# Kernel optimization log

Measured on AMD Instinct MI355X. Metric: run time of the kernel, lower is better.

## Reference

```python
import jax, jax.numpy as jnp
import numpy as np

NEG = -1e30  # log-space 'zero' (avoids -inf NaN issues under jit)
EPS = 1e-7   # keras.backend.epsilon()


def _ctc_loss(y_true, y_pred):
    # y_true: [B, L] int labels in [0, C-1), y_pred: [B, T, C] softmax probs.
    # Keras ctc_batch_cost: logits = log(y_pred + eps), then tf.nn.ctc_loss
    # (which applies log_softmax internally), blank = C - 1.
    B, T, C = y_pred.shape
    L = y_true.shape[1]
    S = 2 * L + 1
    blank = C - 1

    logp = jax.nn.log_softmax(jnp.log(y_pred + EPS), axis=-1)  # [B, T, C]

    # Extended label sequence: blank, l1, blank, l2, ..., blank  -> [B, S]
    ext = jnp.full((B, S), blank, dtype=y_true.dtype).at[:, 1::2].set(y_true)
    lp_ext = jnp.take_along_axis(logp, ext[:, None, :].astype(jnp.int32), axis=2)  # [B, T, S]

    # skip transition s-2 -> s allowed iff ext[s] != blank and ext[s] != ext[s-2]
    ext_m2 = jnp.concatenate([jnp.full((B, 2), blank, ext.dtype), ext[:, :-2]], axis=1)
    allow_skip = (ext != blank) & (ext != ext_m2)
    allow_skip = allow_skip.at[:, :2].set(False)

    # alpha init at t=0
    alpha = jnp.full((B, S), NEG, dtype=logp.dtype)
    alpha = alpha.at[:, 0].set(lp_ext[:, 0, 0]).at[:, 1].set(lp_ext[:, 0, 1])

    neg1 = jnp.full((B, 1), NEG, dtype=logp.dtype)
    neg2 = jnp.full((B, 2), NEG, dtype=logp.dtype)

    def step(a, lp_t):
        prev1 = jnp.concatenate([neg1, a[:, :-1]], axis=1)
        prev2 = jnp.concatenate([neg2, a[:, :-2]], axis=1)
        acc = jnp.logaddexp(a, prev1)
        acc = jnp.where(allow_skip, jnp.logaddexp(acc, prev2), acc)
        return acc + lp_t, None

    lp_seq = jnp.transpose(lp_ext, (1, 0, 2))[1:]  # [T-1, B, S]
    alpha, _ = jax.lax.scan(step, alpha, lp_seq)

    loss = -jnp.logaddexp(alpha[:, -1], alpha[:, -2])  # [B]
    return loss[:, None]  # [B, 1] like keras ctc_batch_cost


def setup_inputs() -> dict:
    key = jax.random.key(0)
    k1, k2 = jax.random.split(key)
    B, T, C, L = 1024, 256, 128, 64
    y_true = jax.random.randint(k1, (B, L), 0, C - 1, dtype=jnp.int32)
    y_pred = jax.random.uniform(k2, (B, T, C), dtype=jnp.float32, minval=1e-4, maxval=1.0)
    return {"y_true": y_true, "y_pred": y_pred}


def reference(y_true, y_pred):
    return _ctc_loss(y_true, y_pred)
```

## Files before the change

kernel.cpp:

```cpp
#include <hip/hip_runtime.h>
#include <math.h>

#define BATCH 1024
#define TT    256
#define CC    128
#define LL    64
#define EPSV  (1e-7f)

typedef float f32x4 __attribute__((ext_vector_type(4)));

template <int CTRL>
__device__ __forceinline__ float dpp0(float x) {
    return __int_as_float(__builtin_amdgcn_update_dpp(0, __float_as_int(x), CTRL, 0xF, 0xF, true));
}
template <int CTRL>
__device__ __forceinline__ float dppS(float x) {
    return __int_as_float(__builtin_amdgcn_update_dpp(__float_as_int(x), __float_as_int(x), CTRL, 0xF, 0xF, false));
}
__device__ __forceinline__ float rol1_f(float x) {
    return __int_as_float(__builtin_amdgcn_update_dpp(__float_as_int(x), __float_as_int(x), 0x134, 0xF, 0xF, false));
}
__device__ __forceinline__ int rol1_i(int x) {
    return __builtin_amdgcn_update_dpp(x, x, 0x134, 0xF, 0xF, false);
}
__device__ __forceinline__ float rdlane(float x, int l) {
    return __int_as_float(__builtin_amdgcn_readlane(__float_as_int(x), l));
}
__device__ __forceinline__ float wave_max_bcast(float m) {
    m = fmaxf(m, dppS<0x111>(m));
    m = fmaxf(m, dppS<0x112>(m));
    m = fmaxf(m, dppS<0x114>(m));
    m = fmaxf(m, dppS<0x118>(m));
    m = fmaxf(m, dppS<0x142>(m));
    m = fmaxf(m, dppS<0x143>(m));
    return rdlane(m, 63);
}
__device__ __forceinline__ unsigned f2h(float x) {
    _Float16 h = (_Float16)x;
    unsigned short u; __builtin_memcpy(&u, &h, 2);
    return (unsigned)u;
}
__device__ __forceinline__ float h2f(unsigned short u) {
    _Float16 h; __builtin_memcpy(&h, &u, 2);
    return (float)h;
}

__global__ __launch_bounds__(512, 8) void ctc_fwd_kernel(const int* __restrict__ y_true,
                                                         const float* __restrict__ y_pred,
                                                         float* __restrict__ out) {
    __shared__ unsigned short qtab[TT][66];
    __shared__ float qblank[TT];
    __shared__ float logZpart[8];

    const int b    = blockIdx.x;
    const int tid  = threadIdx.x;
    const int wv   = tid >> 6;
    const int lane = tid & 63;

    const float* yp = y_pred + (size_t)b * (TT * CC);
    const int lab  = y_true[b * LL + lane];
    const int srcA = lab >> 2;
    const int srcB = 32 + srcA;
    const bool hiPair = (lab & 2) != 0;
    const bool hiHalf = (lab & 1) != 0;

    const int off = ((lane >> 5) << 7) + ((lane & 31) << 2);
    const float* base = yp + off;

    float zacc = 0.0f;
    f32x4 v[4];
    #pragma unroll
    for (int j = 0; j < 4; ++j)
        v[j] = __builtin_nontemporal_load((const f32x4*)(base + 256 * (wv + 8 * j)));

    for (int g = 0; g < 4; ++g) {
        f32x4 vn[4];
        if (g < 3) {
            #pragma unroll
            for (int j = 0; j < 4; ++j)
                vn[j] = __builtin_nontemporal_load((const f32x4*)(base + 256 * (wv + 32 * (g + 1) + 8 * j)));
        }
        #pragma unroll
        for (int j = 0; j < 4; ++j) {
            const int r2 = wv + 32 * g + 8 * j;
            const int tA = 2 * r2, tB = tA + 1;
            float q0 = v[j][0] + EPSV, q1 = v[j][1] + EPSV;
            float q2 = v[j][2] + EPSV, q3 = v[j][3] + EPSV;
            float s = (q0 + q1) + (q2 + q3);
            s += dpp0<0x111>(s);
            s += dpp0<0x112>(s);
            s += dpp0<0x114>(s);
            s += dpp0<0x118>(s);
            s += dpp0<0x142>(s);
            zacc += __logf(s);
            int i01 = (int)(f2h(q0) | (f2h(q1) << 16));
            int i23 = (int)(f2h(q2) | (f2h(q3) << 16));
            int gA01 = __shfl(i01, srcA), gA23 = __shfl(i23, srcA);
            int gB01 = __shfl(i01, srcB), gB23 = __shfl(i23, srcB);
            int sA = hiPair ? gA23 : gA01;
            int sB = hiPair ? gB23 : gB01;
            qtab[tA][lane] = (unsigned short)(hiHalf ? ((unsigned)sA >> 16) : (sA & 0xFFFF));
            qtab[tB][lane] = (unsigned short)(hiHalf ? ((unsigned)sB >> 16) : (sB & 0xFFFF));
            if ((lane & 31) == 31) qblank[tA + (lane >> 5)] = q3;
        }
        #pragma unroll
        for (int j = 0; j < 4; ++j) v[j] = vn[j];
    }
    {
        float z31 = rdlane(zacc, 31), z63 = rdlane(zacc, 63);
        if (lane == 0) logZpart[wv] = z31 + z63;
    }
    __syncthreads();

    if (wv == 0) {
        float logZ = 0.0f;
        #pragma unroll
        for (int w = 0; w < 8; ++w) logZ += logZpart[w];

        const int labm1  = rol1_i(lab);
        const float mskip = (lane >= 1 && lab != labm1) ? 1.0f : 0.0f;
        const bool l0 = (lane == 0);

        float a0 = l0 ? qblank[0] : 0.0f;
        float a1 = l0 ? h2f(qtab[0][lane]) : 0.0f;
        float aX = 0.0f;
        int Esum = 0;

        float qbv[8], qlv[8];
        #pragma unroll
        for (int i = 0; i < 8; ++i) {
            qbv[i] = qblank[1 + i];
            qlv[i] = h2f(qtab[1 + i][lane]);
        }

        for (int t0 = 1; t0 + 8 <= TT; t0 += 8) {
            float qbn[8], qln[8];
            #pragma unroll
            for (int i = 0; i < 8; ++i) {
                int tn = t0 + 8 + i; tn = (tn < TT) ? tn : (TT - 1);
                qbn[i] = qblank[tn];
                qln[i] = h2f(qtab[tn][lane]);
            }
            #pragma unroll
            for (int i = 0; i < 8; ++i) {
                float nb  = rol1_f(a1);
                float na0 = (a0 + (l0 ? 0.0f : nb)) * qbv[i];
                float na1 = fmaf(mskip, nb, a0 + a1) * qlv[i];
                aX = l0 ? (aX + nb) * qbv[i] : 0.0f;
                a0 = na0; a1 = na1;
            }
            float m = fmaxf(fmaxf(a0, a1), aX);
            float mall = wave_max_bcast(m);
            int ex = (int)((__float_as_uint(mall) >> 23) & 0xFF);
            int e  = 127 - ex;
            float sc = __uint_as_float((unsigned)(127 + e) << 23);
            a0 *= sc; a1 *= sc; aX *= sc;
            Esum += e;
            #pragma unroll
            for (int i = 0; i < 8; ++i) { qbv[i] = qbn[i]; qlv[i] = qln[i]; }
        }
        #pragma unroll
        for (int i = 0; i < 7; ++i) {
            float nb  = rol1_f(a1);
            float na0 = (a0 + (l0 ? 0.0f : nb)) * qbv[i];
            float na1 = fmaf(mskip, nb, a0 + a1) * qlv[i];
            aX = l0 ? (aX + nb) * qbv[i] : 0.0f;
            a0 = na0; a1 = na1;
        }
        float a127 = rdlane(a1, 63);
        if (lane == 0) {
            float tot = aX + a127;
            out[b] = logZ + (float)Esum * 0.69314718055994531f - __logf(tot);
        }
    }
}

extern "C" void kernel_launch(void* const* d_in, const int* in_sizes, int n_in,
                              void* d_out, int out_size, void* d_ws, size_t ws_size,
                              hipStream_t stream) {
    const int*   y_true = (const int*)d_in[0];
    const float* y_pred = (const float*)d_in[1];
    float*       out    = (float*)d_out;
    ctc_fwd_kernel<<<BATCH, 512, 0, stream>>>(y_true, y_pred, out);
}
```

Before: 37.38 us.

## Overlap CTC recursion with producer waves via LDS chunk counters

Makes wave 0 a dedicated consumer that runs the alpha recursion while waves 1-7 load y_pred, build the fp16 label-probability table and signal per-chunk completion through LDS atomic counters. Wave 0 spins on each 8-timestep chunk instead of waiting at one block-wide barrier, so the serial recursion starts before the load phase finishes. It also swaps the per-element fp16 conversion for packed cvt_pkrtz. The risks are spin-wait overhead, relying on LDS ordering through waitcnt and atomics, one fewer loading wave, and round-toward-zero conversion changing rounding slightly.

```diff
diff --git a/kernel.cpp b/kernel.cpp
--- a/kernel.cpp
+++ b/kernel.cpp
@@ -8,6 +8,7 @@
 #define EPSV  (1e-7f)
 
 typedef float f32x4 __attribute__((ext_vector_type(4)));
+typedef __fp16 fp16x2 __attribute__((ext_vector_type(2)));
 
 template <int CTRL>
 __device__ __forceinline__ float dpp0(float x) {
@@ -35,10 +36,10 @@
     m = fmaxf(m, dppS<0x143>(m));
     return rdlane(m, 63);
 }
-__device__ __forceinline__ unsigned f2h(float x) {
-    _Float16 h = (_Float16)x;
-    unsigned short u; __builtin_memcpy(&u, &h, 2);
-    return (unsigned)u;
+__device__ __forceinline__ int pkrtz(float a, float b) {
+    fp16x2 h = __builtin_amdgcn_cvt_pkrtz(a, b);
+    int r; __builtin_memcpy(&r, &h, 4);
+    return r;
 }
 __device__ __forceinline__ float h2f(unsigned short u) {
     _Float16 h; __builtin_memcpy(&h, &u, 2);
@@ -51,6 +52,8 @@
     __shared__ unsigned short qtab[TT][66];
     __shared__ float qblank[TT];
     __shared__ float logZpart[8];
+    __shared__ int   chunkCnt[32];
+    __shared__ int   doneCnt;
 
     const int b    = blockIdx.x;
     const int tid  = threadIdx.x;
@@ -67,110 +70,124 @@
     const int off = ((lane >> 5) << 7) + ((lane & 31) << 2);
     const float* base = yp + off;
 
-    float zacc = 0.0f;
-    f32x4 v[4];
-    #pragma unroll
-    for (int j = 0; j < 4; ++j)
-        v[j] = __builtin_nontemporal_load((const f32x4*)(base + 256 * (wv + 8 * j)));
-
-    for (int g = 0; g < 4; ++g) {
-        f32x4 vn[4];
-        if (g < 3) {
-            #pragma unroll
-            for (int j = 0; j < 4; ++j)
-                vn[j] = __builtin_nontemporal_load((const f32x4*)(base + 256 * (wv + 32 * (g + 1) + 8 * j)));
-        }
+    if (tid < 32) chunkCnt[tid] = 0;
+    if (tid == 32) doneCnt = 0;
+    __syncthreads();
+
+    if (wv > 0) {
+        const int sw = wv - 1;
+        float zacc = 0.0f;
+        f32x4 v[8];
         #pragma unroll
-        for (int j = 0; j < 4; ++j) {
-            const int r2 = wv + 32 * g + 8 * j;
+        for (int d = 0; d < 8; ++d) {
+            int r2 = sw + 7 * d; r2 = (r2 < 128) ? r2 : 127;
+            v[d] = *(const f32x4*)(base + 256 * r2);
+        }
+        #pragma unroll
+        for (int i = 0; i < 19; ++i) {
+            const int  r2i   = sw + 7 * i;
+            const bool valid = (r2i < 128);
+            const int  r2    = valid ? r2i : 127;
+            f32x4 x = v[i & 7];
+            if (i + 8 < 19) {
+                int rn = sw + 7 * (i + 8); rn = (rn < 128) ? rn : 127;
+                v[i & 7] = *(const f32x4*)(base + 256 * rn);
+            }
             const int tA = 2 * r2, tB = tA + 1;
-            float q0 = v[j][0] + EPSV, q1 = v[j][1] + EPSV;
-            float q2 = v[j][2] + EPSV, q3 = v[j][3] + EPSV;
+            float q0 = x[0] + EPSV, q1 = x[1] + EPSV;
+            float q2 = x[2] + EPSV, q3 = x[3] + EPSV;
             float s = (q0 + q1) + (q2 + q3);
             s += dpp0<0x111>(s);
             s += dpp0<0x112>(s);
             s += dpp0<0x114>(s);
             s += dpp0<0x118>(s);
             s += dpp0<0x142>(s);
-            zacc += __logf(s);
-            int i01 = (int)(f2h(q0) | (f2h(q1) << 16));
-            int i23 = (int)(f2h(q2) | (f2h(q3) << 16));
+            if (valid) zacc += __logf(s);
+            int i01 = pkrtz(q0, q1);
+            int i23 = pkrtz(q2, q3);
             int gA01 = __shfl(i01, srcA), gA23 = __shfl(i23, srcA);
             int gB01 = __shfl(i01, srcB), gB23 = __shfl(i23, srcB);
             int sA = hiPair ? gA23 : gA01;
             int sB = hiPair ? gB23 : gB01;
-            qtab[tA][lane] = (unsigned short)(hiHalf ? ((unsigned)sA >> 16) : (sA & 0xFFFF));
-            qtab[tB][lane] = (unsigned short)(hiHalf ? ((unsigned)sB >> 16) : (sB & 0xFFFF));
-            if ((lane & 31) == 31) qblank[tA + (lane >> 5)] = q3;
-        }
-        #pragma unroll
-        for (int j = 0; j < 4; ++j) v[j] = vn[j];
-    }
-    {
+            if (valid) {
+                qtab[tA][lane] = (unsigned short)(hiHalf ? ((unsigned)sA >> 16) : (sA & 0xFFFF));
+                qtab[tB][lane] = (unsigned short)(hiHalf ? ((unsigned)sB >> 16) : (sB & 0xFFFF));
+                if ((lane & 31) == 31) qblank[tA + (lane >> 5)] = q3;
+                asm volatile("s_waitcnt lgkmcnt(0)" ::: "memory");
+                if (lane == 0) atomicAdd(&chunkCnt[r2 >> 2], 1);
+            }
+        }
         float z31 = rdlane(zacc, 31), z63 = rdlane(zacc, 63);
-        if (lane == 0) logZpart[wv] = z31 + z63;
-    }
-    __syncthreads();
-
-    if (wv == 0) {
-        float logZ = 0.0f;
-        #pragma unroll
-        for (int w = 0; w < 8; ++w) logZ += logZpart[w];
-
-        const int labm1  = rol1_i(lab);
+        if (lane == 0) {
+            logZpart[wv] = z31 + z63;
+            asm volatile("s_waitcnt lgkmcnt(0)" ::: "memory");
+            atomicAdd(&doneCnt, 1);
+        }
+    } else {
+        const int   labm1 = rol1_i(lab);
         const float mskip = (lane >= 1 && lab != labm1) ? 1.0f : 0.0f;
-        const bool l0 = (lane == 0);
+        const bool  l0 = (lane == 0);
+
+        volatile int* vcnt = chunkCnt;
+        while (vcnt[0] < 4) __builtin_amdgcn_s_sleep(1);
+        __builtin_amdgcn_sched_barrier(0);
 
         float a0 = l0 ? qblank[0] : 0.0f;
         float a1 = l0 ? h2f(qtab[0][lane]) : 0.0f;
         float aX = 0.0f;
         int Esum = 0;
 
-        float qbv[8], qlv[8];
-        #pragma unroll
-        for (int i = 0; i < 8; ++i) {
-            qbv[i] = qblank[1 + i];
-            qlv[i] = h2f(qtab[1 + i][lane]);
-        }
-
-        for (int t0 = 1; t0 + 8 <= TT; t0 += 8) {
-            float qbn[8], qln[8];
-            #pragma unroll
-            for (int i = 0; i < 8; ++i) {
-                int tn = t0 + 8 + i; tn = (tn < TT) ? tn : (TT - 1);
-                qbn[i] = qblank[tn];
-                qln[i] = h2f(qtab[tn][lane]);
-            }
-            #pragma unroll
-            for (int i = 0; i < 8; ++i) {
+        {
+            float qb8[8], ql8[8];
+            #pragma unroll
+            for (int i = 1; i < 8; ++i) { qb8[i] = qblank[i]; ql8[i] = h2f(qtab[i][lane]); }
+            #pragma unroll
+            for (int i = 1; i < 8; ++i) {
                 float nb  = rol1_f(a1);
-                float na0 = (a0 + (l0 ? 0.0f : nb)) * qbv[i];
-                float na1 = fmaf(mskip, nb, a0 + a1) * qlv[i];
-                aX = l0 ? (aX + nb) * qbv[i] : 0.0f;
+                float na0 = (a0 + (l0 ? 0.0f : nb)) * qb8[i];
+                float na1 = fmaf(mskip, nb, a0 + a1) * ql8[i];
+                aX = l0 ? (aX + nb) * qb8[i] : 0.0f;
                 a0 = na0; a1 = na1;
             }
-            float m = fmaxf(fmaxf(a0, a1), aX);
-            float mall = wave_max_bcast(m);
-            int ex = (int)((__float_as_uint(mall) >> 23) & 0xFF);
-            int e  = 127 - ex;
+            float mall = wave_max_bcast(fmaxf(fmaxf(a0, a1), aX));
+            int e = 127 - (int)((__float_as_uint(mall) >> 23) & 0xFF);
             float sc = __uint_as_float((unsigned)(127 + e) << 23);
             a0 *= sc; a1 *= sc; aX *= sc;
             Esum += e;
-            #pragma unroll
-            for (int i = 0; i < 8; ++i) { qbv[i] = qbn[i]; qlv[i] = qln[i]; }
-        }
+        }
+        for (int c = 1; c < 32; ++c) {
+            while (vcnt[c] < 4) __builtin_amdgcn_s_sleep(1);
+            __builtin_amdgcn_sched_barrier(0);
+            float qb8[8], ql8[8];
+            #pragma unroll
+            for (int i = 0; i < 8; ++i) {
+                const int t = 8 * c + i;
+                qb8[i] = qblank[t];
+                ql8[i] = h2f(qtab[t][lane]);
+            }
+            #pragma unroll
+            for (int i = 0; i < 8; ++i) {
+                float nb  = rol1_f(a1);
+                float na0 = (a0 + (l0 ? 0.0f : nb)) * qb8[i];
+                float na1 = fmaf(mskip, nb, a0 + a1) * ql8[i];
+                aX = l0 ? (aX + nb) * qb8[i] : 0.0f;
+                a0 = na0; a1 = na1;
+            }
+            float mall = wave_max_bcast(fmaxf(fmaxf(a0, a1), aX));
+            int e = 127 - (int)((__float_as_uint(mall) >> 23) & 0xFF);
+            float sc = __uint_as_float((unsigned)(127 + e) << 23);
+            a0 *= sc; a1 *= sc; aX *= sc;
+            Esum += e;
+        }
+        volatile int* vd = &doneCnt;
+        while (*vd < 7) __builtin_amdgcn_s_sleep(1);
+        __builtin_amdgcn_sched_barrier(0);
+        float LZ = 0.0f;
         #pragma unroll
-        for (int i = 0; i < 7; ++i) {
-            float nb  = rol1_f(a1);
-            float na0 = (a0 + (l0 ? 0.0f : nb)) * qbv[i];
-            float na1 = fmaf(mskip, nb, a0 + a1) * qlv[i];
-            aX = l0 ? (aX + nb) * qbv[i] : 0.0f;
-            a0 = na0; a1 = na1;
-        }
+        for (int w = 1; w < 8; ++w) LZ += logZpart[w];
         float a127 = rdlane(a1, 63);
         if (lane == 0) {
-            float tot = aX + a127;
-            out[b] = logZ + (float)Esum * 0.69314718055994531f - __logf(tot);
+            out[b] = LZ + (float)Esum * 0.69314718055994531f - __logf(aX + a127);
         }
     }
 }
```

After: 37.26 us. Within noise of the previous version (-0.3%).
